# Kernel optimization log

Measured on AMD Instinct MI355X. Metric: run time of the kernel, lower is better.

Reference implementation:

```python
import jax, jax.numpy as jnp
import numpy as np

H = 128
N0 = 32768
N1 = 32768
N = N0 + N1
E = 524288
R = 4
L = 2
BS = 1024
PER = N // BS


def setup_inputs() -> dict:
    key = jax.random.key(0)
    ks = jax.random.split(key, 20)
    s = 1.0 / np.sqrt(H)
    x0 = jax.random.normal(ks[0], (N0, H), jnp.float32)
    x1 = jax.random.normal(ks[1], (N1, H), jnp.float32)
    W0 = jax.random.normal(ks[2], (H, H), jnp.float32) * s
    W1 = jax.random.normal(ks[3], (H, H), jnp.float32) * s
    conv_root = jax.random.normal(ks[4], (L, H, H), jnp.float32) * s
    conv_rel = jax.random.normal(ks[5], (L, R, H, H), jnp.float32) * s
    attW = jax.random.normal(ks[6], (L, R * R, H, H), jnp.float32) * s
    att_q = jax.random.normal(ks[7], (L, R * R, H), jnp.float32) * s
    att_k = jax.random.normal(ks[8], (L, R * R, H), jnp.float32) * s
    fc_W = jax.random.normal(ks[9], (H, H), jnp.float32) * s
    src = jax.random.randint(ks[10], (E,), 0, N)
    dst = jax.random.randint(ks[11], (E,), 0, N)
    edge_index = jnp.stack([src, dst], 0)
    edge_type = jax.random.randint(ks[12], (E,), 0, R)
    # mask: ones, but zero the first node of ~half the samples (mirrors torch.rand(batch)<0.5)
    drop = jax.random.uniform(ks[13], (BS,)) < 0.5
    row_mask = jnp.where(drop[:, None, None] & (jnp.arange(PER)[None, :, None] == 0), 0.0, 1.0)
    mask = jnp.broadcast_to(row_mask, (BS, PER, H)).reshape(N, H).astype(jnp.float32)
    return {
        "x0": x0, "x1": x1, "W0": W0, "b0": jnp.zeros((H,), jnp.float32),
        "W1": W1, "b1": jnp.zeros((H,), jnp.float32), "mask": mask,
        "conv_root": conv_root, "conv_rel": conv_rel, "conv_b": jnp.zeros((L, H), jnp.float32),
        "attW": attW, "att_q": att_q, "att_k": att_k, "att_b": jnp.zeros((L, H), jnp.float32),
        "bn_g": jnp.ones((L, H), jnp.float32), "bn_b": jnp.zeros((L, H), jnp.float32),
        "fc_W": fc_W, "fc_b": jnp.zeros((H,), jnp.float32),
        "edge_index": edge_index, "edge_type": edge_type, "batch_size": BS,
    }


def reference(x0, x1, W0, b0, W1, b1, mask, conv_root, conv_rel, conv_b,
              attW, att_q, att_k, att_b, bn_g, bn_b, fc_W, fc_b,
              edge_index, edge_type, batch_size):
    n = x0.shape[0] + x1.shape[0]
    r = conv_rel.shape[1]
    # per-node-type linear transforms, then to_homogeneous concat
    x_in = jnp.concatenate([x0 @ W0 + b0, x1 @ W1 + b1], axis=0)  # [N,H]
    src, dst = edge_index[0], edge_index[1]
    seg = dst * r + edge_type  # (target node, relation) segments
    x = x_in
    for l in range(conv_root.shape[0]):
        xm = x * mask
        # ---- RGCNConv: per-relation transform, mean aggregation per relation, root + bias
        xr = jnp.einsum('nh,rho->rno', xm, conv_rel[l])  # [R,N,H]
        m = xr[edge_type, src]  # [E,H]
        s = jax.ops.segment_sum(m, seg, num_segments=n * r)
        cnt = jax.ops.segment_sum(jnp.ones((seg.shape[0],), m.dtype), seg, num_segments=n * r)
        agg = (s / jnp.maximum(cnt, 1.0)[:, None]).reshape(n, r, -1).sum(1)
        x_conv = agg + xm @ conv_root[l] + conv_b[l]
        # ---- RGATConv (heads=1, within-relation softmax, additive self-attention)
        xa = jnp.einsum('nh,rho->rno', xm, attW[l, :r])  # only real edge types used
        sq = jnp.einsum('rnh,rh->rn', xa, att_q[l, :r])
        sk = jnp.einsum('rnh,rh->rn', xa, att_k[l, :r])
        logit = jax.nn.leaky_relu(sq[edge_type, dst] + sk[edge_type, src], 0.2)  # [E]
        mx = jax.ops.segment_max(logit, seg, num_segments=n * r)
        mx = jnp.where(jnp.isfinite(mx), mx, 0.0)
        ex = jnp.exp(logit - mx[seg])
        den = jax.ops.segment_sum(ex, seg, num_segments=n * r)
        alpha = ex / jnp.maximum(den[seg], 1e-16)
        x_att = jax.ops.segment_sum(alpha[:, None] * xa[edge_type, src], dst, num_segments=n) + att_b[l]
        # ---- BatchNorm (training stats) + leaky_relu(0.01)
        h = x_conv + x_att
        mu = h.mean(0)
        var = h.var(0)
        h = (h - mu) / jnp.sqrt(var + 1e-5) * bn_g[l] + bn_b[l]
        x = jax.nn.leaky_relu(h, 0.01)
    out = (x + x_in) @ fc_W + fc_b
    out = out.reshape(batch_size, -1, out.shape[-1])
    return out[:, 0], out[:, 1:, :]
```

## Files before the change

kernel.cpp:

```cpp
#include <hip/hip_runtime.h>

#define Hd 128
#define NTOT 65536
#define RREL 4
#define NRSEG (NTOT*RREL)
#define NEDGE 524288

typedef unsigned short u16;
typedef unsigned int u32;
typedef short bf16x8 __attribute__((ext_vector_type(8)));
typedef float f32x4 __attribute__((ext_vector_type(4)));

__device__ __forceinline__ u16 f2bf(float f) {
  u32 u = __float_as_uint(f);
  return (u16)((u + 0x7fffu + ((u >> 16) & 1u)) >> 16);
}
__device__ __forceinline__ u32 pack2(float lo, float hi) {
  return ((u32)f2bf(hi) << 16) | f2bf(lo);
}

__device__ __forceinline__ int swzb(int row, int o) {
  return (row*256 + o) ^ ((row & 15) << 4);
}

__device__ __forceinline__ void stage_tile(const u16* __restrict__ g, int ld,
                                           u16* lds, int wave, int lane) {
#pragma unroll
  for (int t = 0; t < 2; ++t) {
    int i = wave*2 + t;
    int row = i*16 + (lane >> 2);
    int col16 = (lane & 3) ^ ((lane >> 3) & 3);
    const u16* src = g + (size_t)row*ld + col16*8;
    __builtin_amdgcn_global_load_lds((const __attribute__((address_space(1))) void*)src,
                                     (__attribute__((address_space(3))) void*)(lds + i*512),
                                     16, 0, 0);
  }
}

template<int CMODE>
__global__ __launch_bounds__(256) void mgemm(const u16* __restrict__ A, int lda,
                                             const u16* __restrict__ Bt, int ldb,
                                             const float* __restrict__ bias,
                                             const float* __restrict__ bias2,
                                             float* __restrict__ C, int kTot)
{
  __shared__ u16 As[4096], Bs[4096];
  const int tid = threadIdx.x, wave = tid >> 6, lane = tid & 63;
  const int wm = wave >> 1, wn = wave & 1;
  int bx = blockIdx.x;
  if (CMODE == 3) {
    if (bx >= (int)gridDim.x/2) {
      bx -= gridDim.x/2;
      A += (size_t)32768*lda; Bt += 128*128; bias = bias2; C += (size_t)32768*Hd;
    }
  }
  const int brow = bx * 128;
  const u16* Ab = A + (size_t)brow*lda;
  f32x4 acc[4][4];
#pragma unroll
  for (int i = 0; i < 4; ++i)
#pragma unroll
    for (int j = 0; j < 4; ++j) acc[i][j] = (f32x4){0.f, 0.f, 0.f, 0.f};

  const int ks = (lane >> 4) * 16;
  const int rl = lane & 15;
  for (int k0 = 0; k0 < kTot; k0 += 32) {
    stage_tile(Ab + k0, lda, As, wave, lane);
    stage_tile(Bt + k0, ldb, Bs, wave, lane);
    __syncthreads();
    bf16x8 af[4], bv[4];
    const char* Ac = (const char*)As;
    const char* Bc = (const char*)Bs;
#pragma unroll
    for (int i = 0; i < 4; ++i) {
      int r = wm*64 + i*16 + rl;
      int by = (r*64 + ks) ^ (((r >> 1) & 3) << 4);
      af[i] = *(const bf16x8*)(Ac + by);
    }
#pragma unroll
    for (int j = 0; j < 4; ++j) {
      int r = wn*64 + j*16 + rl;
      int by = (r*64 + ks) ^ (((r >> 1) & 3) << 4);
      bv[j] = *(const bf16x8*)(Bc + by);
    }
#pragma unroll
    for (int i = 0; i < 4; ++i)
#pragma unroll
      for (int j = 0; j < 4; ++j)
        acc[i][j] = __builtin_amdgcn_mfma_f32_16x16x32_bf16(af[i], bv[j], acc[i][j], 0, 0, 0);
    __syncthreads();
  }
  const int cl = lane & 15;
  const int rq = (lane >> 4) * 4;
#pragma unroll
  for (int i = 0; i < 4; ++i) {
#pragma unroll
    for (int q = 0; q < 4; ++q) {
      int row = brow + wm*64 + i*16 + rq + q;
      size_t ob;
      if (CMODE == 2) {
        int b = row >> 6, p = row & 63;
        ob = (p == 0) ? (size_t)b*Hd
                      : (size_t)(1024*Hd) + ((size_t)(b*63 + (p-1)))*Hd;
      } else {
        ob = (size_t)row * Hd;
      }
#pragma unroll
      for (int j = 0; j < 4; ++j) {
        int col = wn*64 + j*16 + cl;
        float v = acc[i][j][q];
        if (bias) v += bias[col];
        C[ob + col] = v;
      }
    }
  }
}

__device__ __forceinline__ void stageB(const u16* __restrict__ gbase, int ld,
                                       u16* lds, int wave, int lane) {
#pragma unroll
  for (int t = 0; t < 4; ++t) {
    int ti = wave*4 + t;
    int row = ti*4 + (lane >> 4);
    int lchunk = (lane & 15) ^ (row & 15);
    const u16* src = gbase + (size_t)row*ld + lchunk*8;
    __builtin_amdgcn_global_load_lds((const __attribute__((address_space(1))) void*)src,
                                     (__attribute__((address_space(3))) void*)(lds + ti*512),
                                     16, 0, 0);
  }
}
__device__ __forceinline__ void stageY32(const u16* __restrict__ gbase, int ld,
                                         u16* lds, int wave, int lane) {
  int row = wave*4 + (lane >> 4);
  int lchunk = (lane & 15) ^ (row & 15);
  const u16* src = gbase + (size_t)row*ld + lchunk*8;
  __builtin_amdgcn_global_load_lds((const __attribute__((address_space(1))) void*)src,
                                   (__attribute__((address_space(3))) void*)(lds + wave*512),
                                   16, 0, 0);
}

__device__ __forceinline__ void mfma32(const u16* Yt, const u16* Bt, f32x4 (&acc)[2],
                                       int wm, int wn, int lane) {
  const int rl = lane & 15;
  const int ko = (lane >> 4) * 16;
  const char* Yc_ = (const char*)Yt;
  const char* Bc_ = (const char*)Bt;
#pragma unroll
  for (int ks = 0; ks < 4; ++ks) {
    int o = ks*64 + ko;
    bf16x8 af = *(const bf16x8*)(Yc_ + swzb(wm*16 + rl, o));
    bf16x8 b0 = *(const bf16x8*)(Bc_ + swzb(wn*32 + rl, o));
    bf16x8 b1 = *(const bf16x8*)(Bc_ + swzb(wn*32 + 16 + rl, o));
    acc[0] = __builtin_amdgcn_mfma_f32_16x16x32_bf16(af, b0, acc[0], 0, 0, 0);
    acc[1] = __builtin_amdgcn_mfma_f32_16x16x32_bf16(af, b1, acc[1], 0, 0, 0);
  }
}

__global__ __launch_bounds__(512, 4) void fused_gemm(
    const u16* __restrict__ xmb, const u32* __restrict__ meta,
    const float* __restrict__ exs, const int* __restrict__ offsets,
    const u16* __restrict__ Btg, float* __restrict__ hbuf, float* __restrict__ bns)
{
  __shared__ u16 Yt[4096];
  __shared__ u16 Bw[16384];
  const int tid = threadIdx.x, wave = tid >> 6, lane = tid & 63;
  const int wm = wave >> 2, wn = wave & 3;
  const int brow = blockIdx.x * 32;
  f32x4 acc[2];
  acc[0] = (f32x4){0.f,0.f,0.f,0.f};
  acc[1] = (f32x4){0.f,0.f,0.f,0.f};

  u32 axp[4];

  for (int r = 0; r < RREL; ++r) {
    const int segBase = (r << 16) + brow;
    __syncthreads();
    stageB(Btg + r*128, 1152, Bw, wave, lane);
#pragma unroll
    for (int g = 0; g < 2; ++g) {
      int ln0 = wave*4 + g*2;
      int e0[2], ct[2];
#pragma unroll
      for (int m = 0; m < 2; ++m) {
        int seg = segBase + ln0 + m;
        e0[m] = offsets[seg];
        ct[m] = offsets[seg+1] - e0[m];
      }
      int   si[2][4];
      float ew[2][4];
#pragma unroll
      for (int m = 0; m < 2; ++m)
#pragma unroll
        for (int k = 0; k < 4; ++k) {
          si[m][k] = (int)(meta[e0[m] + k] & 0xffffu);
          ew[m][k] = exs[e0[m] + k];
        }
      u32 uu[2][4];
#pragma unroll
      for (int m = 0; m < 2; ++m)
#pragma unroll
        for (int k = 0; k < 4; ++k) {
          int sx = (k < ct[m]) ? si[m][k] : 0;
          uu[m][k] = *(const u32*)(xmb + ((size_t)sx << 7) + lane*2);
        }
      float cx[2], cy[2], ax[2], ay[2];
#pragma unroll
      for (int m = 0; m < 2; ++m) { cx[m] = cy[m] = ax[m] = ay[m] = 0.f; }
#pragma unroll
      for (int m = 0; m < 2; ++m) {
#pragma unroll
        for (int k = 0; k < 4; ++k) {
          float pr = (k < ct[m]) ? 1.f : 0.f;
          float al = pr * ew[m][k];
          float vx = __uint_as_float(uu[m][k] << 16);
          float vy = __uint_as_float(uu[m][k] & 0xffff0000u);
          cx[m] = fmaf(pr, vx, cx[m]);
          cy[m] = fmaf(pr, vy, cy[m]);
          ax[m] = fmaf(al, vx, ax[m]);
          ay[m] = fmaf(al, vy, ay[m]);
        }
        for (int e = e0[m] + 4; e < e0[m] + ct[m]; ++e) {
          int s = (int)(meta[e] & 0xffffu);
          float al = exs[e];
          u32 u = *(const u32*)(xmb + ((size_t)s << 7) + lane*2);
          float vx = __uint_as_float(u << 16);
          float vy = __uint_as_float(u & 0xffff0000u);
          cx[m] += vx; cy[m] += vy;
          ax[m] = fmaf(al, vx, ax[m]);
          ay[m] = fmaf(al, vy, ay[m]);
        }
      }
#pragma unroll
      for (int m = 0; m < 2; ++m) {
        int ln = ln0 + m;
        float ic = 1.f / (float)max(ct[m], 1);
        *(u32*)((char*)Yt + swzb(ln, lane*4)) = pack2(cx[m]*ic, cy[m]*ic);
        axp[g*2+m] = pack2(ax[m], ay[m]);
      }
    }
    __syncthreads();
    mfma32(Yt, Bw, acc, wm, wn, lane);
    __syncthreads();
    stageB(Btg + (4+r)*128, 1152, Bw, wave, lane);
#pragma unroll
    for (int g = 0; g < 2; ++g)
#pragma unroll
      for (int m = 0; m < 2; ++m) {
        int ln = wave*4 + g*2 + m;
        *(u32*)((char*)Yt + swzb(ln, lane*4)) = axp[g*2+m];
      }
    __syncthreads();
    mfma32(Yt, Bw, acc, wm, wn, lane);
  }
  __syncthreads();
  stageY32(xmb + ((size_t)brow << 7), Hd, Yt, wave, lane);
  stageB(Btg + 8*128, 1152, Bw, wave, lane);
  __syncthreads();
  mfma32(Yt, Bw, acc, wm, wn, lane);

  const int cl = lane & 15, rq = (lane >> 4) * 4;
#pragma unroll
  for (int j = 0; j < 2; ++j) {
    float s = 0.f, s2 = 0.f;
#pragma unroll
    for (int q = 0; q < 4; ++q) {
      float v = acc[j][q];
      int row = brow + wm*16 + rq + q;
      hbuf[(size_t)row*Hd + wn*32 + j*16 + cl] = v;
      s += v; s2 = fmaf(v, v, s2);
    }
    s  += __shfl_xor(s, 16);  s  += __shfl_xor(s, 32);
    s2 += __shfl_xor(s2, 16); s2 += __shfl_xor(s2, 32);
    if (lane < 16) {
      int col = wn*32 + j*16 + cl;
      unsafeAtomicAdd(&bns[col], s);
      unsafeAtomicAdd(&bns[128 + col], s2);
    }
  }
}

__global__ void wtrans_all(const float* __restrict__ conv_rel, const float* __restrict__ attW,
                           const float* __restrict__ conv_root, const float* __restrict__ W0,
                           const float* __restrict__ W1, const float* __restrict__ fcW,
                           u16* __restrict__ Btg0, u16* __restrict__ Btg1, u16* __restrict__ Btw) {
  int idx = blockIdx.x*256 + threadIdx.x;
  if (idx < 294912) {
    int l = idx / 147456;
    int rem = idx - l*147456;
    u16* Btg = l ? Btg1 : Btg0;
    float v; int o, kk;
    if (rem < 65536)       { o = rem & 127; kk = rem >> 7;               v = conv_rel[(size_t)l*65536 + rem]; }
    else if (rem < 131072) { int r2 = rem - 65536; o = r2 & 127; kk = 512 + (r2 >> 7); v = attW[(size_t)l*262144 + r2]; }
    else                   { int r3 = rem - 131072; o = r3 & 127; kk = 1024 + (r3 >> 7); v = conv_root[(size_t)l*16384 + r3]; }
    Btg[(size_t)o*1152 + kk] = f2bf(v);
  } else {
    int rem = idx - 294912;
    int w = rem >> 14, r3 = rem & 16383;
    int k = r3 >> 7, o = r3 & 127;
    const float* sp = (w == 0) ? W0 : (w == 1 ? W1 : fcW);
    Btw[w*16384 + o*128 + k] = f2bf(sp[r3]);
  }
}

__global__ void fill_i32(int* p, int v, int n) {
  int i = blockIdx.x*blockDim.x + threadIdx.x;
  if (i < n) p[i] = v;
}
__global__ void rowmask_k(const float* __restrict__ mask, float* __restrict__ rm) {
  int n = blockIdx.x*blockDim.x + threadIdx.x;
  if (n < NTOT) rm[n] = mask[(size_t)n*Hd];
}
__global__ void edge_count(const int* __restrict__ dst, const int* __restrict__ et, int* __restrict__ cnt) {
  int e = blockIdx.x*blockDim.x + threadIdx.x;
  if (e < NEDGE) atomicAdd(&cnt[(et[e] << 16) + dst[e]], 1);
}
__global__ void cvt_bf16_2(const float* __restrict__ s0, const float* __restrict__ s1,
                           u16* __restrict__ dst) {
  int i = blockIdx.x*256 + threadIdx.x;
  const int half = 32768*Hd/4;
  const float* s = (i < half) ? s0 : s1;
  int ii = (i < half) ? i : i - half;
  float4 v = *reinterpret_cast<const float4*>(s + (size_t)ii*4);
  *reinterpret_cast<uint2*>(dst + (size_t)i*4) = make_uint2(pack2(v.x, v.y), pack2(v.z, v.w));
}

__global__ void scan1_k(const int* __restrict__ cnt, int* __restrict__ partial, int* __restrict__ bsum) {
  __shared__ int sh[256];
  int t = threadIdx.x;
  int i = blockIdx.x*256 + t;
  int v = cnt[i];
  sh[t] = v; __syncthreads();
  for (int off = 1; off < 256; off <<= 1) {
    int u = (t >= off) ? sh[t-off] : 0;
    __syncthreads();
    sh[t] += u;
    __syncthreads();
  }
  partial[i] = sh[t] - v;
  if (t == 255) bsum[blockIdx.x] = sh[255];
}
__global__ void scan2_k(int* __restrict__ bsum) {
  __shared__ int sh[256];
  int t = threadIdx.x;
  int v0 = bsum[t*4+0], v1 = bsum[t*4+1], v2 = bsum[t*4+2], v3 = bsum[t*4+3];
  int tot = v0+v1+v2+v3;
  sh[t] = tot; __syncthreads();
  for (int off = 1; off < 256; off <<= 1) {
    int u = (t >= off) ? sh[t-off] : 0;
    __syncthreads();
    sh[t] += u;
    __syncthreads();
  }
  int base = sh[t] - tot;
  bsum[t*4+0] = base;
  bsum[t*4+1] = base + v0;
  bsum[t*4+2] = base + v0+v1;
  bsum[t*4+3] = base + v0+v1+v2;
}
__global__ void scan3_k(const int* __restrict__ partial, const int* __restrict__ bsum, int* __restrict__ offsets) {
  int i = blockIdx.x*256 + threadIdx.x;
  offsets[i] = partial[i] + bsum[i >> 8];
  if (i == 0) offsets[NRSEG] = NEDGE;
}
__global__ void csr_fill(const int* __restrict__ src, const int* __restrict__ dst,
                         const int* __restrict__ et, const int* __restrict__ offsets,
                         int* __restrict__ fillctr, u32* __restrict__ meta) {
  int e = blockIdx.x*blockDim.x + threadIdx.x;
  if (e >= NEDGE) return;
  int d = dst[e];
  int seg = (et[e] << 16) + d;
  int pos = offsets[seg] + atomicAdd(&fillctr[seg], 1);
  meta[pos] = (u32)src[e] | ((u32)d << 16);
}

__global__ void qkvec_all(const float* __restrict__ attW, const float* __restrict__ att_q,
                          const float* __restrict__ att_k,
                          float* __restrict__ qvecL, float* __restrict__ kvecL) {
  int l = blockIdx.x;
  const float* aW = attW + (size_t)l*16*Hd*Hd;
  const float* aq = att_q + (size_t)l*16*Hd;
  const float* ak = att_k + (size_t)l*16*Hd;
  int r = threadIdx.x >> 7, h = threadIdx.x & 127;
  const float* wrow = aW + ((size_t)r*Hd + h)*Hd;
  const float* qv = aq + (size_t)r*Hd;
  const float* kv = ak + (size_t)r*Hd;
  float sq_ = 0.f, sk_ = 0.f;
  for (int o = 0; o < Hd; ++o) { float w = wrow[o]; sq_ = fmaf(w, qv[o], sq_); sk_ = fmaf(w, kv[o], sk_); }
  qvecL[l*512 + r*Hd + h] = sq_;
  kvecL[l*512 + r*Hd + h] = sk_;
}

template<int MODE>
__global__ __launch_bounds__(256) void xform_sqk(
    const float* __restrict__ hin, const float* __restrict__ scale,
    const float* __restrict__ shift, const float* __restrict__ rm,
    const float* __restrict__ x_in, const float* __restrict__ qvec,
    const float* __restrict__ kvec, u16* __restrict__ xmb,
    float* __restrict__ sq, float* __restrict__ sk)
{
  int n = blockIdx.x*4 + (threadIdx.x >> 6);
  int lane = threadIdx.x & 63;
  float2 v = *(const float2*)(hin + (size_t)n*Hd + lane*2);
  if (MODE != 0) {
    float2 sc = *(const float2*)(scale + lane*2);
    float2 sh = *(const float2*)(shift + lane*2);
    v.x = fmaf(v.x, sc.x, sh.x); v.y = fmaf(v.y, sc.y, sh.y);
    v.x = v.x >= 0.f ? v.x : 0.01f*v.x;
    v.y = v.y >= 0.f ? v.y : 0.01f*v.y;
  }
  float2 xb;
  if (MODE == 2) {
    float2 rs = *(const float2*)(x_in + (size_t)n*Hd + lane*2);
    xb.x = v.x + rs.x; xb.y = v.y + rs.y;
  } else {
    float s = rm[n];
    xb.x = v.x*s; xb.y = v.y*s;
  }
  *(u32*)(xmb + (size_t)n*Hd + lane*2) = pack2(xb.x, xb.y);
  if (MODE != 2) {
    float pq[RREL], pk[RREL];
#pragma unroll
    for (int r = 0; r < RREL; ++r) {
      float2 q = *(const float2*)(qvec + r*Hd + lane*2);
      float2 k = *(const float2*)(kvec + r*Hd + lane*2);
      pq[r] = xb.x*q.x + xb.y*q.y;
      pk[r] = xb.x*k.x + xb.y*k.y;
    }
#pragma unroll
    for (int off = 32; off > 0; off >>= 1)
#pragma unroll
      for (int r = 0; r < RREL; ++r) {
        pq[r] += __shfl_xor(pq[r], off);
        pk[r] += __shfl_xor(pk[r], off);
      }
    if (lane == 0)
#pragma unroll
      for (int r = 0; r < RREL; ++r) {
        sq[(size_t)r*NTOT + n] = pq[r];
        sk[(size_t)r*NTOT + n] = pk[r];
      }
  }
}

__global__ void seg_alpha(const u32* __restrict__ meta, const int* __restrict__ offsets,
                          const float* __restrict__ sq, const float* __restrict__ sk,
                          float* __restrict__ exs, float* __restrict__ bns) {
  int seg = blockIdx.x*256 + threadIdx.x;
  if (blockIdx.x == 0 && threadIdx.x < 256) bns[threadIdx.x] = 0.f;
  int e0 = offsets[seg], e1 = offsets[seg+1];
  if (e0 == e1) return;
  const float* skr = sk + (seg & 0xFFFF0000u);
  float sqv = sq[seg];
  float sum = 0.f;
  for (int e = e0; e < e1; ++e) {
    float lg = sqv + skr[meta[e] & 0xffff];
    lg = lg >= 0.f ? lg : 0.2f*lg;
    float ex = __expf(lg);
    exs[e] = ex;
    sum += ex;
  }
  float inv = 1.f / fmaxf(sum, 1e-16f);
  for (int e = e0; e < e1; ++e) exs[e] *= inv;
}

__global__ void bn_final(const float* __restrict__ bns, const float* __restrict__ g,
                         const float* __restrict__ b, float* __restrict__ scale,
                         float* __restrict__ shift) {
  int c = threadIdx.x;
  float mu = bns[c] * (1.f/NTOT);
  float var = bns[128 + c] * (1.f/NTOT) - mu*mu;
  float sc = g[c] / sqrtf(var + 1e-5f);
  scale[c] = sc;
  shift[c] = b[c] - mu*sc;
}

extern "C" void kernel_launch(void* const* d_in, const int* in_sizes, int n_in,
                              void* d_out, int out_size, void* d_ws, size_t ws_size,
                              hipStream_t stream) {
  const float* x0       = (const float*)d_in[0];
  const float* x1       = (const float*)d_in[1];
  const float* W0       = (const float*)d_in[2];
  const float* b0       = (const float*)d_in[3];
  const float* W1       = (const float*)d_in[4];
  const float* b1       = (const float*)d_in[5];
  const float* mask     = (const float*)d_in[6];
  const float* conv_root= (const float*)d_in[7];
  const float* conv_rel = (const float*)d_in[8];
  const float* attW     = (const float*)d_in[10];
  const float* att_q    = (const float*)d_in[11];
  const float* att_k    = (const float*)d_in[12];
  const float* bn_g     = (const float*)d_in[14];
  const float* bn_b     = (const float*)d_in[15];
  const float* fc_W     = (const float*)d_in[16];
  const float* fc_b     = (const float*)d_in[17];
  const int* edge_index = (const int*)d_in[18];
  const int* edge_type  = (const int*)d_in[19];
  const int* src = edge_index;
  const int* dst = edge_index + NEDGE;
  (void)in_sizes; (void)n_in; (void)out_size; (void)ws_size;

  char* ws = (char*)d_ws;
  size_t off = 0;
  auto alloc = [&](size_t bytes) { void* p = ws + off; off = (off + bytes + 255) & ~(size_t)255; return p; };
  float* x_in  = (float*)alloc((size_t)NTOT*Hd*4);
  float* hbuf  = (float*)alloc((size_t)NTOT*Hd*4);
  u16*   xmb   = (u16*)  alloc((size_t)NTOT*Hd*2);
  float* sq    = (float*)alloc((size_t)RREL*NTOT*4);
  float* sk    = (float*)alloc((size_t)RREL*NTOT*4);
  float* exs   = (float*)alloc((size_t)(NEDGE+16)*4);
  float* rm    = (float*)alloc((size_t)NTOT*4);
  int* cnt     = (int*)alloc((size_t)NRSEG*4);
  int* fillctr = (int*)alloc((size_t)NRSEG*4);
  int* partial = (int*)alloc((size_t)NRSEG*4);
  int* offsets = (int*)alloc((size_t)(NRSEG+4)*4);
  int* bsum    = (int*)alloc(4096);
  u32* meta    = (u32*)alloc((size_t)(NEDGE+16)*4);
  float* qvecL = (float*)alloc(2*512*4);
  float* kvecL = (float*)alloc(2*512*4);
  float* bns    = (float*)alloc(1024);
  float* bnscale= (float*)alloc(512);
  float* bnshift= (float*)alloc(512);
  u16* Btw  = (u16*)alloc((size_t)3*128*128*2);
  u16* Btg0 = (u16*)alloc((size_t)128*1152*2);
  u16* Btg1 = (u16*)alloc((size_t)128*1152*2);
  u16* BtgL[2] = {Btg0, Btg1};

  rowmask_k<<<NTOT/256, 256, 0, stream>>>(mask, rm);
  fill_i32<<<NRSEG/256, 256, 0, stream>>>(cnt, 0, NRSEG);
  edge_count<<<NEDGE/256, 256, 0, stream>>>(dst, edge_type, cnt);
  scan1_k<<<NRSEG/256, 256, 0, stream>>>(cnt, partial, bsum);
  scan2_k<<<1, 256, 0, stream>>>(bsum);
  scan3_k<<<NRSEG/256, 256, 0, stream>>>(partial, bsum, offsets);
  fill_i32<<<NRSEG/256, 256, 0, stream>>>(fillctr, 0, NRSEG);
  csr_fill<<<NEDGE/256, 256, 0, stream>>>(src, dst, edge_type, offsets, fillctr, meta);

  wtrans_all<<<1344, 256, 0, stream>>>(conv_rel, attW, conv_root, W0, W1, fc_W,
                                       Btg0, Btg1, Btw);
  qkvec_all<<<2, 512, 0, stream>>>(attW, att_q, att_k, qvecL, kvecL);

  cvt_bf16_2<<<(NTOT*Hd/4)/256, 256, 0, stream>>>(x0, x1, xmb);
  mgemm<3><<<512, 256, 0, stream>>>(xmb, Hd, Btw, 128, b0, b1, x_in, 128);
  xform_sqk<0><<<NTOT/4, 256, 0, stream>>>(x_in, nullptr, nullptr, rm, nullptr,
                                           qvecL, kvecL, xmb, sq, sk);

  for (int l = 0; l < 2; ++l) {
    seg_alpha<<<NRSEG/256, 256, 0, stream>>>(meta, offsets, sq, sk, exs, bns);
    fused_gemm<<<NTOT/32, 512, 0, stream>>>(xmb, meta, exs, offsets, BtgL[l], hbuf, bns);
    bn_final<<<1, 128, 0, stream>>>(bns, bn_g + (size_t)l*Hd, bn_b + (size_t)l*Hd, bnscale, bnshift);
    if (l == 0)
      xform_sqk<1><<<NTOT/4, 256, 0, stream>>>(hbuf, bnscale, bnshift, rm, nullptr,
                                               qvecL + 512, kvecL + 512, xmb, sq, sk);
    else
      xform_sqk<2><<<NTOT/4, 256, 0, stream>>>(hbuf, bnscale, bnshift, nullptr, x_in,
                                               nullptr, nullptr, xmb, sq, sk);
  }

  mgemm<2><<<512, 256, 0, stream>>>(xmb, Hd, Btw + 2*16384, 128, fc_b, nullptr,
                                    (float*)d_out, 128);
}
```

Before: 502.9 us.

## Fuse attention softmax into aggregation GEMM and enlarge row tile to 64

```diff
diff --git a/kernel.cpp b/kernel.cpp
--- a/kernel.cpp
+++ b/kernel.cpp
@@ -129,17 +129,21 @@
                                      16, 0, 0);
   }
 }
-__device__ __forceinline__ void stageY32(const u16* __restrict__ gbase, int ld,
+__device__ __forceinline__ void stageY64(const u16* __restrict__ gbase, int ld,
                                          u16* lds, int wave, int lane) {
-  int row = wave*4 + (lane >> 4);
-  int lchunk = (lane & 15) ^ (row & 15);
-  const u16* src = gbase + (size_t)row*ld + lchunk*8;
-  __builtin_amdgcn_global_load_lds((const __attribute__((address_space(1))) void*)src,
-                                   (__attribute__((address_space(3))) void*)(lds + wave*512),
-                                   16, 0, 0);
-}
-
-__device__ __forceinline__ void mfma32(const u16* Yt, const u16* Bt, f32x4 (&acc)[2],
+#pragma unroll
+  for (int t = 0; t < 2; ++t) {
+    int ti = wave*2 + t;
+    int row = ti*4 + (lane >> 4);
+    int lchunk = (lane & 15) ^ (row & 15);
+    const u16* src = gbase + (size_t)row*ld + lchunk*8;
+    __builtin_amdgcn_global_load_lds((const __attribute__((address_space(1))) void*)src,
+                                     (__attribute__((address_space(3))) void*)(lds + ti*512),
+                                     16, 0, 0);
+  }
+}
+
+__device__ __forceinline__ void mfma64(const u16* Yt, const u16* Bt, f32x4 (&acc)[2][2],
                                        int wm, int wn, int lane) {
   const int rl = lane & 15;
   const int ko = (lane >> 4) * 16;
@@ -148,70 +152,85 @@
 #pragma unroll
   for (int ks = 0; ks < 4; ++ks) {
     int o = ks*64 + ko;
-    bf16x8 af = *(const bf16x8*)(Yc_ + swzb(wm*16 + rl, o));
-    bf16x8 b0 = *(const bf16x8*)(Bc_ + swzb(wn*32 + rl, o));
-    bf16x8 b1 = *(const bf16x8*)(Bc_ + swzb(wn*32 + 16 + rl, o));
-    acc[0] = __builtin_amdgcn_mfma_f32_16x16x32_bf16(af, b0, acc[0], 0, 0, 0);
-    acc[1] = __builtin_amdgcn_mfma_f32_16x16x32_bf16(af, b1, acc[1], 0, 0, 0);
-  }
-}
-
-__global__ __launch_bounds__(512, 4) void fused_gemm(
+    bf16x8 af[2], bv[2];
+#pragma unroll
+    for (int i = 0; i < 2; ++i)
+      af[i] = *(const bf16x8*)(Yc_ + swzb(wm*32 + i*16 + rl, o));
+#pragma unroll
+    for (int j = 0; j < 2; ++j)
+      bv[j] = *(const bf16x8*)(Bc_ + swzb(wn*32 + j*16 + rl, o));
+#pragma unroll
+    for (int i = 0; i < 2; ++i)
+#pragma unroll
+      for (int j = 0; j < 2; ++j)
+        acc[i][j] = __builtin_amdgcn_mfma_f32_16x16x32_bf16(af[i], bv[j], acc[i][j], 0, 0, 0);
+  }
+}
+
+__global__ __launch_bounds__(512, 2) void fused_gemm(
     const u16* __restrict__ xmb, const u32* __restrict__ meta,
-    const float* __restrict__ exs, const int* __restrict__ offsets,
-    const u16* __restrict__ Btg, float* __restrict__ hbuf, float* __restrict__ bns)
+    const int* __restrict__ offsets, const float* __restrict__ sq,
+    const float* __restrict__ sk, const u16* __restrict__ Btg,
+    float* __restrict__ hbuf, float* __restrict__ bns)
 {
-  __shared__ u16 Yt[4096];
+  __shared__ u16 Yt[8192];
   __shared__ u16 Bw[16384];
   const int tid = threadIdx.x, wave = tid >> 6, lane = tid & 63;
   const int wm = wave >> 2, wn = wave & 3;
-  const int brow = blockIdx.x * 32;
-  f32x4 acc[2];
-  acc[0] = (f32x4){0.f,0.f,0.f,0.f};
-  acc[1] = (f32x4){0.f,0.f,0.f,0.f};
-
-  u32 axp[4];
+  const int brow = blockIdx.x * 64;
+  f32x4 acc[2][2];
+#pragma unroll
+  for (int i = 0; i < 2; ++i)
+#pragma unroll
+    for (int j = 0; j < 2; ++j) acc[i][j] = (f32x4){0.f,0.f,0.f,0.f};
+
+  u32 axp[8];
 
   for (int r = 0; r < RREL; ++r) {
     const int segBase = (r << 16) + brow;
+    const float* skr = sk + ((size_t)r << 16);
     __syncthreads();
     stageB(Btg + r*128, 1152, Bw, wave, lane);
 #pragma unroll
-    for (int g = 0; g < 2; ++g) {
-      int ln0 = wave*4 + g*2;
+    for (int g = 0; g < 4; ++g) {
+      int ln0 = wave*8 + g*2;
       int e0[2], ct[2];
+      float sqv[2];
 #pragma unroll
       for (int m = 0; m < 2; ++m) {
         int seg = segBase + ln0 + m;
         e0[m] = offsets[seg];
         ct[m] = offsets[seg+1] - e0[m];
-      }
-      int   si[2][4];
-      float ew[2][4];
+        sqv[m] = sq[seg];
+      }
+      int s_[2][4];
 #pragma unroll
       for (int m = 0; m < 2; ++m)
 #pragma unroll
+        for (int k = 0; k < 4; ++k)
+          s_[m][k] = (int)(meta[e0[m] + k] & 0xffffu);
+      float ex[2][4];
+      u32 uu[2][4];
+#pragma unroll
+      for (int m = 0; m < 2; ++m)
+#pragma unroll
         for (int k = 0; k < 4; ++k) {
-          si[m][k] = (int)(meta[e0[m] + k] & 0xffffu);
-          ew[m][k] = exs[e0[m] + k];
-        }
-      u32 uu[2][4];
-#pragma unroll
-      for (int m = 0; m < 2; ++m)
-#pragma unroll
-        for (int k = 0; k < 4; ++k) {
-          int sx = (k < ct[m]) ? si[m][k] : 0;
+          float lg = sqv[m] + skr[s_[m][k]];
+          lg = lg >= 0.f ? lg : 0.2f*lg;
+          ex[m][k] = __expf(lg);
+          int sx = (k < ct[m]) ? s_[m][k] : 0;
           uu[m][k] = *(const u32*)(xmb + ((size_t)sx << 7) + lane*2);
         }
-      float cx[2], cy[2], ax[2], ay[2];
-#pragma unroll
-      for (int m = 0; m < 2; ++m) { cx[m] = cy[m] = ax[m] = ay[m] = 0.f; }
+      float cx[2], cy[2], ax[2], ay[2], den[2];
+#pragma unroll
+      for (int m = 0; m < 2; ++m) { cx[m]=cy[m]=ax[m]=ay[m]=den[m]=0.f; }
 #pragma unroll
       for (int m = 0; m < 2; ++m) {
 #pragma unroll
         for (int k = 0; k < 4; ++k) {
           float pr = (k < ct[m]) ? 1.f : 0.f;
-          float al = pr * ew[m][k];
+          float al = pr * ex[m][k];
+          den[m] += al;
           float vx = __uint_as_float(uu[m][k] << 16);
           float vy = __uint_as_float(uu[m][k] & 0xffff0000u);
           cx[m] = fmaf(pr, vx, cx[m]);
@@ -221,53 +240,60 @@
         }
         for (int e = e0[m] + 4; e < e0[m] + ct[m]; ++e) {
           int s = (int)(meta[e] & 0xffffu);
-          float al = exs[e];
+          float lg = sqv[m] + skr[s];
+          lg = lg >= 0.f ? lg : 0.2f*lg;
+          float exv = __expf(lg);
+          den[m] += exv;
           u32 u = *(const u32*)(xmb + ((size_t)s << 7) + lane*2);
           float vx = __uint_as_float(u << 16);
           float vy = __uint_as_float(u & 0xffff0000u);
           cx[m] += vx; cy[m] += vy;
-          ax[m] = fmaf(al, vx, ax[m]);
-          ay[m] = fmaf(al, vy, ay[m]);
+          ax[m] = fmaf(exv, vx, ax[m]);
+          ay[m] = fmaf(exv, vy, ay[m]);
         }
       }
 #pragma unroll
       for (int m = 0; m < 2; ++m) {
         int ln = ln0 + m;
         float ic = 1.f / (float)max(ct[m], 1);
+        float idn = 1.f / fmaxf(den[m], 1e-16f);
         *(u32*)((char*)Yt + swzb(ln, lane*4)) = pack2(cx[m]*ic, cy[m]*ic);
-        axp[g*2+m] = pack2(ax[m], ay[m]);
-      }
-    }
-    __syncthreads();
-    mfma32(Yt, Bw, acc, wm, wn, lane);
+        axp[g*2+m] = pack2(ax[m]*idn, ay[m]*idn);
+      }
+    }
+    __syncthreads();
+    mfma64(Yt, Bw, acc, wm, wn, lane);
     __syncthreads();
     stageB(Btg + (4+r)*128, 1152, Bw, wave, lane);
 #pragma unroll
-    for (int g = 0; g < 2; ++g)
+    for (int g = 0; g < 4; ++g)
 #pragma unroll
       for (int m = 0; m < 2; ++m) {
-        int ln = wave*4 + g*2 + m;
+        int ln = wave*8 + g*2 + m;
         *(u32*)((char*)Yt + swzb(ln, lane*4)) = axp[g*2+m];
       }
     __syncthreads();
-    mfma32(Yt, Bw, acc, wm, wn, lane);
+    mfma64(Yt, Bw, acc, wm, wn, lane);
   }
   __syncthreads();
-  stageY32(xmb + ((size_t)brow << 7), Hd, Yt, wave, lane);
+  stageY64(xmb + ((size_t)brow << 7), Hd, Yt, wave, lane);
   stageB(Btg + 8*128, 1152, Bw, wave, lane);
   __syncthreads();
-  mfma32(Yt, Bw, acc, wm, wn, lane);
+  mfma64(Yt, Bw, acc, wm, wn, lane);
 
   const int cl = lane & 15, rq = (lane >> 4) * 4;
 #pragma unroll
   for (int j = 0; j < 2; ++j) {
     float s = 0.f, s2 = 0.f;
 #pragma unroll
-    for (int q = 0; q < 4; ++q) {
-      float v = acc[j][q];
-      int row = brow + wm*16 + rq + q;
-      hbuf[(size_t)row*Hd + wn*32 + j*16 + cl] = v;
-      s += v; s2 = fmaf(v, v, s2);
+    for (int i = 0; i < 2; ++i) {
+#pragma unroll
+      for (int q = 0; q < 4; ++q) {
+        float v = acc[i][j][q];
+        int row = brow + wm*32 + i*16 + rq + q;
+        hbuf[(size_t)row*Hd + wn*32 + j*16 + cl] = v;
+        s += v; s2 = fmaf(v, v, s2);
+      }
     }
     s  += __shfl_xor(s, 16);  s  += __shfl_xor(s, 32);
     s2 += __shfl_xor(s2, 16); s2 += __shfl_xor(s2, 32);
@@ -306,10 +332,6 @@
   int i = blockIdx.x*blockDim.x + threadIdx.x;
   if (i < n) p[i] = v;
 }
-__global__ void rowmask_k(const float* __restrict__ mask, float* __restrict__ rm) {
-  int n = blockIdx.x*blockDim.x + threadIdx.x;
-  if (n < NTOT) rm[n] = mask[(size_t)n*Hd];
-}
 __global__ void edge_count(const int* __restrict__ dst, const int* __restrict__ et, int* __restrict__ cnt) {
   int e = blockIdx.x*blockDim.x + threadIdx.x;
   if (e < NEDGE) atomicAdd(&cnt[(et[e] << 16) + dst[e]], 1);
@@ -393,11 +415,12 @@
 template<int MODE>
 __global__ __launch_bounds__(256) void xform_sqk(
     const float* __restrict__ hin, const float* __restrict__ scale,
-    const float* __restrict__ shift, const float* __restrict__ rm,
+    const float* __restrict__ shift, const float* __restrict__ mask,
     const float* __restrict__ x_in, const float* __restrict__ qvec,
     const float* __restrict__ kvec, u16* __restrict__ xmb,
-    float* __restrict__ sq, float* __restrict__ sk)
+    float* __restrict__ sq, float* __restrict__ sk, float* __restrict__ bns)
 {
+  if (MODE != 2 && blockIdx.x == 0) bns[threadIdx.x] = 0.f;
   int n = blockIdx.x*4 + (threadIdx.x >> 6);
   int lane = threadIdx.x & 63;
   float2 v = *(const float2*)(hin + (size_t)n*Hd + lane*2);
@@ -413,7 +436,7 @@
     float2 rs = *(const float2*)(x_in + (size_t)n*Hd + lane*2);
     xb.x = v.x + rs.x; xb.y = v.y + rs.y;
   } else {
-    float s = rm[n];
+    float s = mask[(size_t)n*Hd];
     xb.x = v.x*s; xb.y = v.y*s;
   }
   *(u32*)(xmb + (size_t)n*Hd + lane*2) = pack2(xb.x, xb.y);
@@ -442,33 +465,14 @@
   }
 }
 
-__global__ void seg_alpha(const u32* __restrict__ meta, const int* __restrict__ offsets,
-                          const float* __restrict__ sq, const float* __restrict__ sk,
-                          float* __restrict__ exs, float* __restrict__ bns) {
-  int seg = blockIdx.x*256 + threadIdx.x;
-  if (blockIdx.x == 0 && threadIdx.x < 256) bns[threadIdx.x] = 0.f;
-  int e0 = offsets[seg], e1 = offsets[seg+1];
-  if (e0 == e1) return;
-  const float* skr = sk + (seg & 0xFFFF0000u);
-  float sqv = sq[seg];
-  float sum = 0.f;
-  for (int e = e0; e < e1; ++e) {
-    float lg = sqv + skr[meta[e] & 0xffff];
-    lg = lg >= 0.f ? lg : 0.2f*lg;
-    float ex = __expf(lg);
-    exs[e] = ex;
-    sum += ex;
-  }
-  float inv = 1.f / fmaxf(sum, 1e-16f);
-  for (int e = e0; e < e1; ++e) exs[e] *= inv;
-}
-
-__global__ void bn_final(const float* __restrict__ bns, const float* __restrict__ g,
+__global__ void bn_final(float* __restrict__ bns, const float* __restrict__ g,
                          const float* __restrict__ b, float* __restrict__ scale,
                          float* __restrict__ shift) {
   int c = threadIdx.x;
-  float mu = bns[c] * (1.f/NTOT);
-  float var = bns[128 + c] * (1.f/NTOT) - mu*mu;
+  float s1 = bns[c], s2 = bns[128 + c];
+  bns[c] = 0.f; bns[128 + c] = 0.f;
+  float mu = s1 * (1.f/NTOT);
+  float var = s2 * (1.f/NTOT) - mu*mu;
   float sc = g[c] / sqrtf(var + 1e-5f);
   scale[c] = sc;
   shift[c] = b[c] - mu*sc;
@@ -507,8 +511,6 @@
   u16*   xmb   = (u16*)  alloc((size_t)NTOT*Hd*2);
   float* sq    = (float*)alloc((size_t)RREL*NTOT*4);
   float* sk    = (float*)alloc((size_t)RREL*NTOT*4);
-  float* exs   = (float*)alloc((size_t)(NEDGE+16)*4);
-  float* rm    = (float*)alloc((size_t)NTOT*4);
   int* cnt     = (int*)alloc((size_t)NRSEG*4);
   int* fillctr = (int*)alloc((size_t)NRSEG*4);
   int* partial = (int*)alloc((size_t)NRSEG*4);
@@ -525,13 +527,11 @@
   u16* Btg1 = (u16*)alloc((size_t)128*1152*2);
   u16* BtgL[2] = {Btg0, Btg1};
 
-  rowmask_k<<<NTOT/256, 256, 0, stream>>>(mask, rm);
-  fill_i32<<<NRSEG/256, 256, 0, stream>>>(cnt, 0, NRSEG);
+  fill_i32<<<2*NRSEG/256, 256, 0, stream>>>(cnt, 0, 2*NRSEG);
   edge_count<<<NEDGE/256, 256, 0, stream>>>(dst, edge_type, cnt);
   scan1_k<<<NRSEG/256, 256, 0, stream>>>(cnt, partial, bsum);
   scan2_k<<<1, 256, 0, stream>>>(bsum);
   scan3_k<<<NRSEG/256, 256, 0, stream>>>(partial, bsum, offsets);
-  fill_i32<<<NRSEG/256, 256, 0, stream>>>(fillctr, 0, NRSEG);
   csr_fill<<<NEDGE/256, 256, 0, stream>>>(src, dst, edge_type, offsets, fillctr, meta);
 
   wtrans_all<<<1344, 256, 0, stream>>>(conv_rel, attW, conv_root, W0, W1, fc_W,
@@ -540,19 +540,18 @@
 
   cvt_bf16_2<<<(NTOT*Hd/4)/256, 256, 0, stream>>>(x0, x1, xmb);
   mgemm<3><<<512, 256, 0, stream>>>(xmb, Hd, Btw, 128, b0, b1, x_in, 128);
-  xform_sqk<0><<<NTOT/4, 256, 0, stream>>>(x_in, nullptr, nullptr, rm, nullptr,
-                                           qvecL, kvecL, xmb, sq, sk);
+  xform_sqk<0><<<NTOT/4, 256, 0, stream>>>(x_in, nullptr, nullptr, mask, nullptr,
+                                           qvecL, kvecL, xmb, sq, sk, bns);
 
   for (int l = 0; l < 2; ++l) {
-    seg_alpha<<<NRSEG/256, 256, 0, stream>>>(meta, offsets, sq, sk, exs, bns);
-    fused_gemm<<<NTOT/32, 512, 0, stream>>>(xmb, meta, exs, offsets, BtgL[l], hbuf, bns);
+    fused_gemm<<<NTOT/64, 512, 0, stream>>>(xmb, meta, offsets, sq, sk, BtgL[l], hbuf, bns);
     bn_final<<<1, 128, 0, stream>>>(bns, bn_g + (size_t)l*Hd, bn_b + (size_t)l*Hd, bnscale, bnshift);
     if (l == 0)
-      xform_sqk<1><<<NTOT/4, 256, 0, stream>>>(hbuf, bnscale, bnshift, rm, nullptr,
-                                               qvecL + 512, kvecL + 512, xmb, sq, sk);
+      xform_sqk<1><<<NTOT/4, 256, 0, stream>>>(hbuf, bnscale, bnshift, mask, nullptr,
+                                               qvecL + 512, kvecL + 512, xmb, sq, sk, bns);
     else
       xform_sqk<2><<<NTOT/4, 256, 0, stream>>>(hbuf, bnscale, bnshift, nullptr, x_in,
-                                               nullptr, nullptr, xmb, sq, sk);
+                                               nullptr, nullptr, xmb, sq, sk, bns);
   }
 
   mgemm<2><<<512, 256, 0, stream>>>(xmb, Hd, Btw + 2*16384, 128, fc_b, nullptr,
```

New measurement: 545.5 us. +8.5%, slower.
